# Optimization experiments

Measured on AMD Instinct MI355X. Metric: run time of the kernel, lower is better.

## Reference

```python
import jax, jax.numpy as jnp
import numpy as np

NEG = 0.2  # LeakyReLU slope

def lrelu(x):
    return jnp.where(x >= 0, x, NEG * x)

def conv2d(x, w, pad):
    return jax.lax.conv_general_dilated(x, w, (1, 1), [(pad, pad), (pad, pad)],
                                        dimension_numbers=('NCHW', 'OIHW', 'NCHW'))

def maxpool2(x):
    return jax.lax.reduce_window(x, -jnp.inf, jax.lax.max, (1, 1, 2, 2), (1, 1, 2, 2), 'VALID')

def batchnorm(x, g, b, eps=1e-5):
    m = jnp.mean(x, axis=(0, 2, 3), keepdims=True)
    v = jnp.var(x, axis=(0, 2, 3), keepdims=True)
    return (x - m) / jnp.sqrt(v + eps) * g[None, :, None, None] + b[None, :, None, None]

def features(x, cw1, bg1, bb1, cw2, bg2, bb2, cw3, bg3, bb3, cw4, bg4, bb4):
    x = maxpool2(lrelu(batchnorm(conv2d(x, cw1, 1), bg1, bb1)))
    x = maxpool2(lrelu(batchnorm(conv2d(x, cw2, 1), bg2, bb2)))
    x = lrelu(batchnorm(conv2d(x, cw3, 1), bg3, bb3))
    x = lrelu(batchnorm(conv2d(x, cw4, 1), bg4, bb4))
    return x  # [B,64,16,16]

def mhsa(x, wq, bq, wk, bk, wv, bv, rel_h, rel_w, ln_g, ln_b, heads=4):
    B, C, W, H = x.shape
    d, hw = C // heads, W * H
    def proj(w, b):
        return (jnp.einsum('oc,bchw->bohw', w, x) + b[None, :, None, None]).reshape(B, heads, d, hw)
    q, k, v = proj(wq, bq), proj(wk, bk), proj(wv, bv)
    cc = jnp.einsum('bhdi,bhdj->bhij', q, k)                 # content-content
    pos = (rel_h + rel_w).reshape(heads, d, hw)              # relative position bias
    cp = jnp.einsum('hdi,bhdj->bhij', pos, q)                # content-position
    attn = jax.nn.softmax(cc + cp, axis=-1)
    out = jnp.einsum('bhdj,bhij->bhdi', v, attn).reshape(B, C, W, H)
    m = jnp.mean(out, axis=(1, 2, 3), keepdims=True)
    va = jnp.var(out, axis=(1, 2, 3), keepdims=True)
    out = (out - m) / jnp.sqrt(va + 1e-5) * ln_g[None] + ln_b[None]
    return out + x

def cbam(x, cw1, cb1, cw2, cb2, sw, sb):
    avg, mx = jnp.mean(x, axis=(2, 3)), jnp.max(x, axis=(2, 3))
    def exc(f):
        return jnp.einsum('oc,bc->bo', cw2, jax.nn.relu(jnp.einsum('oc,bc->bo', cw1, f) + cb1)) + cb2
    x = jax.nn.sigmoid(exc(avg) + exc(mx))[:, :, None, None] * x
    sf = jnp.stack([jnp.mean(x, axis=1), jnp.max(x, axis=1)], axis=1)  # [B,2,H,W]
    sa = jax.nn.sigmoid(conv2d(sf, sw, 3) + sb[None, :, None, None])
    return sa * x

def sa_module(x, mh, cb):
    return mhsa(x, *mh) + cbam(x, *cb) + x

def setup_inputs() -> dict:
    key = jax.random.key(0)
    ks = jax.random.split(key, 24)
    rn = lambda k, s, sc=1.0: jax.random.normal(k, s, dtype=jnp.float32) * sc
    inp = {
        'input1': rn(ks[0], (64, 1, 64, 64)),
        'input2': rn(ks[1], (5, 5, 1, 64, 64)),
        'conv1_w': rn(ks[2], (64, 1, 3, 3), 0.3),
        'bn1_g': jnp.ones(64), 'bn1_b': jnp.zeros(64),
        'conv2_w': rn(ks[3], (64, 64, 3, 3), 0.05),
        'bn2_g': jnp.ones(64), 'bn2_b': jnp.zeros(64),
        'conv3_w': rn(ks[4], (64, 64, 3, 3), 0.05),
        'bn3_g': jnp.ones(64), 'bn3_b': jnp.zeros(64),
        'conv4_w': rn(ks[5], (64, 64, 3, 3), 0.05),
        'bn4_g': jnp.ones(64), 'bn4_b': jnp.zeros(64),
        'wq': rn(ks[6], (64, 64), 0.12), 'bq': rn(ks[7], (64,), 0.01),
        'wk': rn(ks[8], (64, 64), 0.12), 'bk': rn(ks[9], (64,), 0.01),
        'wv': rn(ks[10], (64, 64), 0.12), 'bv': rn(ks[11], (64,), 0.01),
        'rel_h': rn(ks[12], (1, 4, 16, 1, 16)),
        'rel_w': rn(ks[13], (1, 4, 16, 16, 1)),
        'ln_g': jnp.ones((64, 16, 16)), 'ln_b': jnp.zeros((64, 16, 16)),
        'ca_w1': rn(ks[14], (4, 64), 0.15), 'ca_b1': jnp.zeros(4),
        'ca_w2': rn(ks[15], (64, 4), 0.15), 'ca_b2': jnp.zeros(64),
        'sa_w': rn(ks[16], (1, 2, 7, 7), 0.1), 'sa_b': jnp.zeros(1),
        'cls_w': rn(ks[17], (256,), 0.05),
    }
    return inp

def reference(input1, input2, conv1_w, bn1_g, bn1_b, conv2_w, bn2_g, bn2_b,
              conv3_w, bn3_g, bn3_b, conv4_w, bn4_g, bn4_b,
              wq, bq, wk, bk, wv, bv, rel_h, rel_w, ln_g, ln_b,
              ca_w1, ca_b1, ca_w2, ca_b2, sa_w, sa_b, cls_w):
    fa = (conv1_w, bn1_g, bn1_b, conv2_w, bn2_g, bn2_b, conv3_w, bn3_g, bn3_b, conv4_w, bn4_g, bn4_b)
    mh = (wq, bq, wk, bk, wv, bv, rel_h, rel_w, ln_g, ln_b)
    cb = (ca_w1, ca_b1, ca_w2, ca_b2, sa_w, sa_b)
    q = sa_module(features(input1, *fa), mh, cb)                      # [B,64,16,16]
    S = jax.vmap(lambda imgs: sa_module(features(imgs, *fa), mh, cb))(input2)  # [ncls,shot,64,16,16]
    ncls, shot = input2.shape[0], input2.shape[1]
    B, C, Hh, Ww = q.shape
    hw = Hh * Ww
    # per-class covariance over channels (CovaBlock.cal_covariance)
    X = S.transpose(0, 2, 1, 3, 4).reshape(ncls, C, shot * hw)
    Xc = X - jnp.mean(X, axis=2, keepdims=True)
    cov = jnp.einsum('ncm,ndm->ncd', Xc, Xc) / (hw * shot - 1)        # [ncls,C,C]
    # query similarity: diag(q^T Cov q) done as fused quadratic form
    Q = q.reshape(B, C, hw)
    Qn = Q / jnp.linalg.norm(Q, axis=2, keepdims=True)
    sim = jnp.einsum('bci,jcd,bdi->bji', Qn, cov, Qn)                 # [B,ncls,hw]
    # classifier: LeakyReLU -> Dropout(eval=identity) -> Conv1d(k=hw, stride=hw, no bias)
    out = jnp.einsum('bjk,k->bj', lrelu(sim), cls_w)
    return out
```

## Files before the change

kernel.cpp:

```cpp
#include <hip/hip_runtime.h>
#include <hip/hip_bf16.h>

__device__ __forceinline__ float lrelu(float x){ return x >= 0.f ? x : 0.2f*x; }
__device__ __forceinline__ float sigm(float x){ return 1.f/(1.f+__expf(-x)); }

typedef short short8 __attribute__((ext_vector_type(8)));
typedef float f32x16 __attribute__((ext_vector_type(16)));

static constexpr size_t OFF_X0    = 0;
static constexpr size_t OFF_POS   = 475712;
static constexpr size_t OFF_WQT   = 492096;
static constexpr size_t OFF_STATS = 504384;
static constexpr size_t OFF_P1    = 507456;
static constexpr size_t OFF_P2    = 7092224;
static constexpr size_t OFF_RES   = 10714688;
static constexpr size_t OFF_MU    = 12172864;
static constexpr size_t OFF_COV   = 12173184;
static constexpr size_t OFF_SIM   = 12193664;
static constexpr size_t OFF_R1    = 12275584;
static constexpr size_t OFF_C2    = OFF_R1;
static constexpr size_t OFF_ATP   = OFF_R1;
static constexpr size_t OFF_C3    = OFF_R1 + 5832704;
static constexpr size_t OFF_C4    = OFF_R1 + 8749056;
static constexpr size_t OFF_CKV   = OFF_R1 + 10207232;
static constexpr size_t OFF_MHRAW = OFF_R1 + 14581760;
static constexpr size_t OFF_QN    = OFF_R1 + 17543680;
static constexpr size_t OFF_WH    = OFF_R1 + 21737984;
static constexpr size_t OFF_WL    = OFF_WH + 18432;

__device__ __forceinline__ int bn_group(int img){ return (img < 64) ? 0 : (1 + (img-64)/5); }

__device__ __forceinline__ void bn_ab(const float* __restrict__ sums, int g, int c, float n,
                                      float gw, float bw, float& a, float& b)
{
    const float sum = sums[(g*64+c)*2], ss = sums[(g*64+c)*2+1];
    const float m = sum/n;
    const float var = fmaxf(ss/n - m*m, 0.f);
    const float istd = 1.f/sqrtf(var + 1e-5f);
    a = gw*istd;
    b = bw - m*a;
}

__global__ __launch_bounds__(256) void prep_k(const float* __restrict__ in1, const float* __restrict__ in2,
        const float* __restrict__ relh, const float* __restrict__ relw,
        const float* __restrict__ wq, const float* __restrict__ wk, const float* __restrict__ wv,
        const float* __restrict__ cw2,
        float* __restrict__ ws)
{
    int idx = blockIdx.x*256 + threadIdx.x;
    if (idx < 364544) { ws[OFF_X0+idx] = (idx < 262144 ? in1[idx] : in2[idx-262144]); return; }
    idx -= 364544;
    if (idx < 16384) {
        const int h = idx>>12, r = idx&4095, i = r>>4, d = r&15;
        ws[OFF_POS+idx] = relh[h*256 + d*16 + (i&15)] + relw[h*256 + d*16 + (i>>4)];
        return;
    }
    idx -= 16384;
    if (idx < 12288) {
        const int s = idx/4096, r = idx%4096, c = r>>6, o = r&63;
        const float* wp = (s==0)?wq:((s==1)?wk:wv);
        ws[OFF_WQT+idx] = wp[o*64 + c];
        return;
    }
    idx -= 12288;
    if (idx < 3072) { ws[OFF_STATS+idx] = 0.f; return; }
    idx -= 3072;
    if (idx < 20480) { ws[OFF_COV+idx] = 0.f; return; }
    idx -= 20480;
    if (idx < 36864) {
        const int och = idx/576, r = idx%576, cin = r/9, k9 = r%9;
        const float v = cw2[idx];
        __hip_bfloat16 hb = __float2bfloat16(v);
        const float hv = __bfloat162float(hb);
        __hip_bfloat16 lb = __float2bfloat16(v - hv);
        unsigned short* WH = (unsigned short*)(ws + OFF_WH);
        unsigned short* WL = (unsigned short*)(ws + OFF_WL);
        const int d = k9*4096 + och*64 + cin;
        WH[d] = *(unsigned short*)&hb;
        WL[d] = *(unsigned short*)&lb;
        return;
    }
    idx -= 36864;
    if (idx < 751872) {
        const int img = idx/8448, r = idx%8448;
        const int pos = r>>6, d = r&63;
        int ypad, xpad;
        if (pos < 68){ ypad = (pos<34)?0:33; xpad = (pos<34)?pos:(pos-34); }
        else { const int q = pos-68; ypad = 1 + (q>>1); xpad = (q&1)*33; }
        ws[OFF_P1 + (((size_t)img*34 + ypad)*34 + xpad)*64 + d] = 0.f;
    }
}

template<int H, int W, int CIN, int CH, int OCB, int PT, bool STORE, bool INBN>
__global__ __launch_bounds__(256) void conv3x3_k(const float* __restrict__ in,
                                                 const float* __restrict__ wt,
                                                 float* __restrict__ out,
                                                 float* __restrict__ bnsum,
                                                 const float* __restrict__ isums,
                                                 const float* __restrict__ igw,
                                                 const float* __restrict__ ibw,
                                                 int ihw)
{
    constexpr int P = W + 1;
    constexpr int PLANE = H * P;
    constexpr int HW = H * W;
    constexpr int PASSES = HW / (256 * PT);
    constexpr int NLD = CH * HW / 256;
    __shared__ float lds[CH * PLANE];
    __shared__ float redS[OCB*4], redQ[OCB*4];
    __shared__ float abA[64], abB[64];
    const int img = blockIdx.x;
    const int och0 = blockIdx.y * OCB;
    const int t = threadIdx.x;

    if constexpr (INBN) {
        if (t < CIN) {
            const int gi = bn_group(img);
            const float nin = (float)(((gi==0)?64:5) * ihw);
            float a, b;
            bn_ab(isums, gi, t, nin, igw[t], ibw[t], a, b);
            abA[t]=a; abB[t]=b;
        }
        __syncthreads();
    }

    float acc[PASSES][OCB][PT];
#pragma unroll
    for (int a=0;a<PASSES;a++)
#pragma unroll
      for (int o=0;o<OCB;o++)
#pragma unroll
        for (int p=0;p<PT;p++) acc[a][o][p]=0.f;

    for (int idx = t; idx < CH*HW; idx += 256) {
        const int c = idx / HW, p = idx % HW;
        float v = in[((size_t)img*CIN + c)*HW + p];
        if constexpr (INBN) v = lrelu(abA[c]*v + abB[c]);
        lds[c*PLANE + (p/W)*P + (p%W)] = v;
    }
    __syncthreads();

    for (int cc0 = 0; cc0 < CIN; cc0 += CH) {
        float pre[(CIN > CH) ? NLD : 1];
        if constexpr (CIN > CH) {
            if (cc0 + CH < CIN) {
#pragma unroll
                for (int j=0;j<NLD;j++){
                    const int idx = j*256 + t;
                    const int c = idx / HW, p = idx % HW;
                    pre[j] = in[((size_t)img*CIN + cc0 + CH + c)*HW + p];
                }
            }
        }
        for (int c = 0; c < CH; ++c) {
            float wr[OCB][9];
#pragma unroll
            for (int o=0;o<OCB;o++)
#pragma unroll
              for (int k=0;k<9;k++)
                wr[o][k] = wt[((size_t)(och0+o)*CIN + (cc0+c))*9 + k];
            const float* Lc = lds + c*PLANE;
#pragma unroll
            for (int ps=0; ps<PASSES; ++ps) {
                const int px0 = (ps*256 + t)*PT;
                const int y = px0 / W, x0 = px0 % W;
#pragma unroll
                for (int ky=0; ky<3; ++ky) {
                    const int yy = y + ky - 1;
                    if (yy >= 0 && yy < H) {
                        const float* Lr = Lc + yy*P;
                        float r[PT+2];
                        r[0] = (x0 > 0) ? Lr[x0-1] : 0.f;
#pragma unroll
                        for (int k2=0;k2<PT;k2++) r[k2+1] = Lr[x0+k2];
                        r[PT+1] = (x0+PT < W) ? Lr[x0+PT] : 0.f;
#pragma unroll
                        for (int p=0;p<PT;p++)
#pragma unroll
                          for (int kx=0;kx<3;kx++) {
                              const float v = r[p+kx];
#pragma unroll
                              for (int o=0;o<OCB;o++)
                                  acc[ps][o][p] += v * wr[o][ky*3+kx];
                          }
                    }
                }
            }
        }
        if constexpr (CIN > CH) {
            if (cc0 + CH < CIN) {
                __syncthreads();
#pragma unroll
                for (int j=0;j<NLD;j++){
                    const int idx = j*256 + t;
                    const int c = idx / HW, p = idx % HW;
                    float v = pre[j];
                    if constexpr (INBN) v = lrelu(abA[cc0+CH+c]*v + abB[cc0+CH+c]);
                    lds[c*PLANE + (p/W)*P + (p%W)] = v;
                }
                __syncthreads();
            }
        }
    }
    if constexpr (STORE) {
#pragma unroll
        for (int ps=0; ps<PASSES; ++ps) {
            const int px0 = (ps*256 + t)*PT;
#pragma unroll
            for (int o=0;o<OCB;o++)
#pragma unroll
              for (int p=0;p<PT;p++)
                out[((size_t)img*64 + och0+o)*HW + px0 + p] = acc[ps][o][p];
        }
    }
    const int g = bn_group(img);
    const int wv = t >> 6;
#pragma unroll
    for (int o=0;o<OCB;o++){
        float s=0.f, ss=0.f;
#pragma unroll
        for (int ps=0;ps<PASSES;ps++)
#pragma unroll
          for (int p=0;p<PT;p++){ const float v=acc[ps][o][p]; s+=v; ss+=v*v; }
#pragma unroll
        for (int off=32; off>0; off>>=1){ s += __shfl_xor(s, off); ss += __shfl_xor(ss, off); }
        if ((t&63)==0){ redS[o*4+wv]=s; redQ[o*4+wv]=ss; }
    }
    __syncthreads();
    if (t < OCB*2){
        const int o = t>>1, metric = t&1;
        const float v = metric ? (redQ[o*4]+redQ[o*4+1]+redQ[o*4+2]+redQ[o*4+3])
                               : (redS[o*4]+redS[o*4+1]+redS[o*4+2]+redS[o*4+3]);
        atomicAdd(&bnsum[(g*64 + och0+o)*2 + metric], v);
    }
}

__global__ __launch_bounds__(256) void bnpoolconv1_k(const float* __restrict__ x0,
        const float* __restrict__ cw, const float* __restrict__ sums,
        const float* __restrict__ gw, const float* __restrict__ bw,
        unsigned short* __restrict__ p1p)
{
    __shared__ float xl[10*64];
    const int img = blockIdx.x, band = blockIdx.y, t = threadIdx.x;
    const int oy0 = band*4;
    const float* xp = x0 + (size_t)img*4096;
    for (int idx=t; idx<640; idx+=256){
        const int iy = idx>>6, ix = idx&63;
        const int gy = 2*oy0 - 1 + iy;
        xl[idx] = (gy>=0 && gy<64) ? xp[gy*64+ix] : 0.f;
    }
    const int g = bn_group(img);
    const float n = (float)(((g==0)?64:5) * 4096);
    __syncthreads();
    const int p = t>>1, half = t&1;
    const int ly = p>>5, ox = p&31;
    float r[4][4];
#pragma unroll
    for (int dy=0;dy<4;dy++){
        const float* Lr = xl + (2*ly+dy)*64;
#pragma unroll
        for (int dx=0;dx<4;dx++){
            const int xx = 2*ox-1+dx;
            r[dy][dx] = (xx>=0 && xx<64) ? Lr[xx] : 0.f;
        }
    }
    short8 hv[4], lv[4];
#pragma unroll
    for (int o=0;o<32;o++){
        const int och = half*32 + o;
        float w[9];
#pragma unroll
        for (int k=0;k<9;k++) w[k] = cw[och*9+k];
        float a, b;
        bn_ab(sums, g, och, n, gw[och], bw[och], a, b);
        float best = -1e30f;
#pragma unroll
        for (int sy=0;sy<2;sy++)
#pragma unroll
          for (int sx=0;sx<2;sx++){
            float s=0.f;
#pragma unroll
            for (int ky=0;ky<3;ky++)
#pragma unroll
              for (int kx=0;kx<3;kx++) s += r[sy+ky][sx+kx]*w[ky*3+kx];
            best = fmaxf(best, lrelu(a*s+b));
          }
        __hip_bfloat16 hb = __float2bfloat16(best);
        const float hf = __bfloat162float(hb);
        __hip_bfloat16 lb = __float2bfloat16(best - hf);
        hv[o>>3][o&7] = (short)*(unsigned short*)&hb;
        lv[o>>3][o&7] = (short)*(unsigned short*)&lb;
    }
    const size_t base = ((((size_t)img*34 + (oy0+ly) + 1)*34) + ox + 1)*128 + half*32;
#pragma unroll
    for (int j=0;j<4;j++){
        *(short8*)(p1p + base + j*8)      = hv[j];
        *(short8*)(p1p + base + 64 + j*8) = lv[j];
    }
}

__global__ __launch_bounds__(256) void conv2mfma_k(const unsigned short* __restrict__ p1p,
        const unsigned short* __restrict__ whi, const unsigned short* __restrict__ wlo,
        float* __restrict__ c2)
{
    __shared__ __align__(16) unsigned short Bx[136*128];
    const int img = blockIdx.x, rowblk = blockIdx.y;
    const int t = threadIdx.x;
    {
        const unsigned short* src = p1p + (((size_t)img*34 + rowblk*2)*34)*128;
        for (int idx=t; idx<2176; idx+=256){
            const int pos = idx>>4, sub = idx&15;
            const short8 v = *(const short8*)(src + pos*128 + sub*8);
            *(short8*)(Bx + pos*128 + ((sub ^ (pos&7))<<3)) = v;
        }
    }
    __syncthreads();
    const int lane = t & 63, wv = t >> 6;
    const int mt = wv & 1, ntp = wv >> 1;
    const int m = lane & 31, kg = lane >> 5;
    f32x16 acc;
#pragma unroll
    for (int r=0;r<16;r++) acc[r]=0.f;

#pragma unroll
    for (int ky=0; ky<3; ky++){
#pragma unroll
      for (int kx=0; kx<3; kx++){
        const int s = ky*3 + kx;
        const unsigned short* wh = whi + ((s*64 + mt*32 + m)<<6) + kg*8;
        const unsigned short* wl = wlo + ((s*64 + mt*32 + m)<<6) + kg*8;
        const int pos = (ntp+ky)*34 + m + kx;
        const int pb  = pos << 7;
        const int sw  = (pos & 7) << 3;
#pragma unroll
        for (int ch=0; ch<4; ch++){
            const short8 ah = *(const short8*)(wh + ch*16);
            const short8 al = *(const short8*)(wl + ch*16);
            const short8 bh = *(const short8*)(Bx + pb + ((ch*16 + (kg<<3)) ^ sw));
            const short8 bl = *(const short8*)(Bx + pb + (64 + ((ch*16 + (kg<<3)) ^ sw)));
            acc = __builtin_amdgcn_mfma_f32_32x32x16_bf16(ah, bh, acc, 0,0,0);
            acc = __builtin_amdgcn_mfma_f32_32x32x16_bf16(al, bh, acc, 0,0,0);
            acc = __builtin_amdgcn_mfma_f32_32x32x16_bf16(ah, bl, acc, 0,0,0);
        }
      }
    }
    const int py = rowblk*2 + ntp;
    float* co = c2 + ((size_t)img*64)*1024 + py*32 + m;
#pragma unroll
    for (int r=0; r<16; r++){
        const int och = mt*32 + (r&3) + 8*(r>>2) + 4*kg;
        co[(size_t)och*1024] = acc[r];
    }
}

__global__ __launch_bounds__(256) void bnstats2_k(const float* __restrict__ in, float* __restrict__ sums)
{
    __shared__ float rs[4], rq[4];
    const int img = blockIdx.x, c = blockIdx.y, t = threadIdx.x;
    const float4 v = ((const float4*)(in + ((size_t)img*64 + c)*1024))[t];
    float s = v.x+v.y+v.z+v.w;
    float q = v.x*v.x+v.y*v.y+v.z*v.z+v.w*v.w;
#pragma unroll
    for (int off=32; off>0; off>>=1){ s += __shfl_xor(s, off); q += __shfl_xor(q, off); }
    if ((t&63)==0){ rs[t>>6]=s; rq[t>>6]=q; }
    __syncthreads();
    if (t==0){
        const int g = bn_group(img);
        atomicAdd(&sums[(g*64+c)*2],   rs[0]+rs[1]+rs[2]+rs[3]);
        atomicAdd(&sums[(g*64+c)*2+1], rq[0]+rq[1]+rq[2]+rq[3]);
    }
}

template<int H, int W>
__global__ __launch_bounds__(256) void bnpool_k(const float* __restrict__ in, const float* __restrict__ sums,
                                 const float* __restrict__ gw, const float* __restrict__ bw,
                                 float* __restrict__ out)
{
    const int img = blockIdx.x, c = blockIdx.y, t = threadIdx.x;
    const int g = bn_group(img);
    const float n = (float)(((g==0)?64:5) * H * W);
    float a, b;
    bn_ab(sums, g, c, n, gw[c], bw[c], a, b);
    constexpr int W2=W/2, HW=H*W, N2=(H/2)*W2;
    const float* pl = in + ((size_t)img*64 + c)*HW;
    float* po = out + ((size_t)img*64 + c)*N2;
    for (int opx=t; opx<N2; opx+=256) {
        const int oy=opx/W2, ox=opx%W2;
        const float* q = pl + (2*oy)*W + 2*ox;
        const float v0=lrelu(a*q[0]+b), v1=lrelu(a*q[1]+b), v2=lrelu(a*q[W]+b), v3=lrelu(a*q[W+1]+b);
        po[opx] = fmaxf(fmaxf(v0,v1),fmaxf(v2,v3));
    }
}

__global__ __launch_bounds__(256) void proj_k(const float* __restrict__ c4, const float* __restrict__ wT,
               const float* __restrict__ bq, const float* __restrict__ bk, const float* __restrict__ bv,
               const float* __restrict__ sums4, const float* __restrict__ gw4, const float* __restrict__ bw4,
               float* __restrict__ ckv)
{
    __shared__ float xl[64*256];
    const int img = blockIdx.x, s = blockIdx.y, t = threadIdx.x;
    const int gi = bn_group(img);
    const float nin = (float)(((gi==0)?64:5) * 256);
    {
        const float4* in4 = (const float4*)(c4 + (size_t)img*16384);
        float4* xl4 = (float4*)xl;
        for (int i=t; i<4096; i+=256){
            float4 v = in4[i];
            const int c = i>>6;
            float a, b;
            bn_ab(sums4, gi, c, nin, gw4[c], bw4[c], a, b);
            v.x=lrelu(a*v.x+b); v.y=lrelu(a*v.y+b); v.z=lrelu(a*v.z+b); v.w=lrelu(a*v.w+b);
            xl4[i] = v;
        }
    }
    const float* bias = (s==0)?bq:((s==1)?bk:bv);
    const int sofs = (s==0)?16:((s==1)?0:32);
    const float* wp = wT + s*4096;
    const int o0 = (t>>4)*4, i0 = (t&15)*16;
    const int h = o0>>4, d0 = o0&15;
    __syncthreads();
    float acc[4][16];
    float b0[4];
#pragma unroll
    for (int o=0;o<4;o++) b0[o]=bias[o0+o];
#pragma unroll
    for (int o=0;o<4;o++)
#pragma unroll
      for (int i=0;i<16;i++) acc[o][i]=b0[o];
    for (int c=0;c<64;c++){
        const float4 w4 = *(const float4*)(wp + c*64 + o0);
        const float* xr = xl + c*256 + i0;
#pragma unroll
        for (int k=0;k<4;k++){
            const float4 x4 = *(const float4*)(xr + 4*k);
            acc[0][4*k+0]+=w4.x*x4.x; acc[0][4*k+1]+=w4.x*x4.y; acc[0][4*k+2]+=w4.x*x4.z; acc[0][4*k+3]+=w4.x*x4.w;
            acc[1][4*k+0]+=w4.y*x4.x; acc[1][4*k+1]+=w4.y*x4.y; acc[1][4*k+2]+=w4.y*x4.z; acc[1][4*k+3]+=w4.y*x4.w;
            acc[2][4*k+0]+=w4.z*x4.x; acc[2][4*k+1]+=w4.z*x4.y; acc[2][4*k+2]+=w4.z*x4.z; acc[2][4*k+3]+=w4.z*x4.w;
            acc[3][4*k+0]+=w4.w*x4.x; acc[3][4*k+1]+=w4.w*x4.y; acc[3][4*k+2]+=w4.w*x4.z; acc[3][4*k+3]+=w4.w*x4.w;
        }
    }
#pragma unroll
    for (int ii=0;ii<16;ii++){
        const float4 v = make_float4(acc[0][ii],acc[1][ii],acc[2][ii],acc[3][ii]);
        *(float4*)(ckv + (((size_t)img*4 + h)*256 + i0+ii)*48 + sofs + d0) = v;
    }
}

__global__ __launch_bounds__(256) void attnp_k(const float* __restrict__ ckv, const float* __restrict__ pos,
                               float* __restrict__ part)
{
    const int img = blockIdx.x, h = blockIdx.y, jc = blockIdx.z, i = threadIdx.x;
    const size_t jb = (((size_t)img*4 + h)*256)*48;
    float areg[32];
    {
        const float* myrow = ckv + jb + (size_t)i*48;
#pragma unroll
        for (int k=0;k<4;k++) *(float4*)&areg[4*k]    = *(const float4*)(myrow + 16 + 4*k);
#pragma unroll
        for (int k=0;k<4;k++) *(float4*)&areg[16+4*k] = *(const float4*)(pos + h*4096 + i*16 + 4*k);
    }
    float mrun = -1e30f, l = 0.f;
    float accv[16];
#pragma unroll
    for (int d=0;d<16;d++) accv[d]=0.f;

    const int jend = jc*64 + 64;
    for (int j0=jc*64; j0<jend; j0+=2){
        const float* r0 = ckv + jb + (size_t)j0*48;
        const float* r1 = r0 + 48;
        float s0a=0.f, s0b=0.f, s1a=0.f, s1b=0.f;
#pragma unroll
        for (int dd=0; dd<16; ++dd){
            s0a += areg[2*dd]  *r0[2*dd];
            s0b += areg[2*dd+1]*r0[2*dd+1];
            s1a += areg[2*dd]  *r1[2*dd];
            s1b += areg[2*dd+1]*r1[2*dd+1];
        }
        const float s0 = s0a+s0b, s1 = s1a+s1b;
        const float mnew = fmaxf(mrun, fmaxf(s0,s1));
        const float al = __expf(mrun - mnew);
        const float e0 = __expf(s0 - mnew), e1 = __expf(s1 - mnew);
        mrun = mnew;
        l = l*al + e0 + e1;
        const float* v0 = r0 + 32;
        const float* v1 = r1 + 32;
#pragma unroll
        for (int d=0;d<16;d++) accv[d] = accv[d]*al + e0*v0[d] + e1*v1[d];
    }
    float* pp = part + ((((size_t)img*4 + h)*4 + jc)*18)*256;
    pp[i]       = mrun;
    pp[256 + i] = l;
#pragma unroll
    for (int d=0;d<16;d++) pp[(2+d)*256 + i] = accv[d];
}

__global__ __launch_bounds__(256) void attnm_k(const float* __restrict__ part, float* __restrict__ mhraw)
{
    const int img = blockIdx.x, h = blockIdx.y, i = threadIdx.x;
    const float* pb = part + (((size_t)img*4 + h)*4*18)*256;
    float mc[4], lc[4];
#pragma unroll
    for (int c=0;c<4;c++){ mc[c] = pb[c*4608 + i]; lc[c] = pb[c*4608 + 256 + i]; }
    const float ms = fmaxf(fmaxf(mc[0],mc[1]), fmaxf(mc[2],mc[3]));
    float wgt[4]; float ls = 0.f;
#pragma unroll
    for (int c=0;c<4;c++){ wgt[c] = __expf(mc[c]-ms); ls += wgt[c]*lc[c]; }
    const float rl = 1.f/ls;
#pragma unroll
    for (int d=0;d<16;d++){
        float v = 0.f;
#pragma unroll
        for (int c=0;c<4;c++) v += wgt[c]*pb[c*4608 + (2+d)*256 + i];
        mhraw[((size_t)img*64 + h*16 + d)*256 + i] = v*rl;
    }
}

__global__ __launch_bounds__(256) void post_k(const float* __restrict__ mhraw,
        const float* __restrict__ lng, const float* __restrict__ lnb,
        const float* __restrict__ c4,
        const float* __restrict__ sums4, const float* __restrict__ gw4, const float* __restrict__ bw4,
        const float* __restrict__ w1, const float* __restrict__ b1,
        const float* __restrict__ w2, const float* __restrict__ b2,
        const float* __restrict__ sw, const float* __restrict__ sb,
        float* __restrict__ res)
{
    __shared__ float r1[256], r2[256];
    __shared__ float favg[64], fmx[64], z1s[8], ca[64];
    __shared__ float sf[512];
    __shared__ float wl[98];
    __shared__ float mh_s[2];
    __shared__ float aA[64], aB[64];
    __shared__ float sa_l[256];
    const int img = blockIdx.x, t = threadIdx.x;
    const float* mb  = mhraw + (size_t)img*16384;
    const float* fbr = c4    + (size_t)img*16384;

    if (t<64){
        const int gi = bn_group(img);
        const float nin = (float)(((gi==0)?64:5) * 256);
        float a, b;
        bn_ab(sums4, gi, t, nin, gw4[t], bw4[t], a, b);
        aA[t]=a; aB[t]=b;
    }
    if (t<98) wl[t] = sw[t];

    {
        const float4* mb4 = (const float4*)mb;
        float s=0.f, ss=0.f;
        for (int i=t; i<4096; i+=256){
            const float4 v = mb4[i];
            s  += v.x+v.y+v.z+v.w;
            ss += v.x*v.x+v.y*v.y+v.z*v.z+v.w*v.w;
        }
        r1[t]=s; r2[t]=ss; __syncthreads();
        for (int st=128;st>0;st>>=1){ if(t<st){r1[t]+=r1[t+st]; r2[t]+=r2[t+st];} __syncthreads(); }
        if (t==0){
            const float m = r1[0]/16384.f;
            const float var = fmaxf(r2[0]/16384.f - m*m, 0.f);
            mh_s[0]=m; mh_s[1]=1.f/sqrtf(var+1e-5f);
        }
    }
    {
        const int c = t>>2, part = t&3;
        const float a = aA[c], b = aB[c];
        const float4* p4 = (const float4*)(fbr + c*256 + part*64);
        float s=0.f, mx=-1e30f;
        for (int k=0;k<16;k++){
            const float4 v = p4[k];
            const float f0=lrelu(a*v.x+b), f1=lrelu(a*v.y+b), f2=lrelu(a*v.z+b), f3=lrelu(a*v.w+b);
            s += f0+f1+f2+f3;
            mx = fmaxf(mx, fmaxf(fmaxf(f0,f1),fmaxf(f2,f3)));
        }
        __syncthreads();
        r1[t]=s; r2[t]=mx;
        __syncthreads();
        if (t<64){
            favg[t] = (r1[t*4]+r1[t*4+1]+r1[t*4+2]+r1[t*4+3])/256.f;
            fmx[t]  = fmaxf(fmaxf(r2[t*4],r2[t*4+1]),fmaxf(r2[t*4+2],r2[t*4+3]));
        }
    }
    __syncthreads();
    if (t<8){
        const int which = t>>2, o = t&3;
        const float* f = which? fmx : favg;
        float z = b1[o];
        for (int c=0;c<64;c++) z += w1[o*64+c]*f[c];
        z1s[t] = fmaxf(z, 0.f);
    }
    __syncthreads();
    if (t<64){
        float z = 2.f*b2[t];
#pragma unroll
        for (int k=0;k<4;k++) z += w2[t*4+k]*(z1s[k]+z1s[4+k]);
        ca[t] = sigm(z);
    }
    __syncthreads();
    {
        float s=0.f, mx=-1e30f;
        for (int c=0;c<64;c++){
            const float fv = lrelu(aA[c]*fbr[c*256+t] + aB[c]);
            const float v = ca[c]*fv;
            s += v; mx = fmaxf(mx, v);
        }
        sf[t]     = s/64.f;
        sf[256+t] = mx;
    }
    __syncthreads();
    {
        float sacc = sb[0];
        const int y = t>>4, x = t&15;
        for (int ch=0; ch<2; ++ch)
          for (int ky=0; ky<7; ++ky){
            const int yy = y+ky-3;
            if (yy<0||yy>=16) continue;
            for (int kx=0; kx<7; ++kx){
                const int xx = x+kx-3;
                if (xx<0||xx>=16) continue;
                sacc += sf[ch*256 + yy*16 + xx]*wl[ch*49 + ky*7 + kx];
            }
          }
        sa_l[t] = sigm(sacc);
    }
    __syncthreads();
    {
        const int q = t & 63;
        const int cb = t >> 6;
        const float m = mh_s[0], istd = mh_s[1];
        const float4* mb4 = (const float4*)mb;
        const float4* fb4 = (const float4*)fbr;
        const float4* lg4 = (const float4*)lng;
        const float4* lb4 = (const float4*)lnb;
        float4* res4 = (float4*)(res + (size_t)img*16384);
        const float sa0=sa_l[4*q], sa1=sa_l[4*q+1], sa2=sa_l[4*q+2], sa3=sa_l[4*q+3];
#pragma unroll 4
        for (int cc=0; cc<16; ++cc){
            const int c = cb*16 + cc;
            const int i4 = c*64 + q;
            const float4 mv = mb4[i4], fv = fb4[i4], gv = lg4[i4], bv = lb4[i4];
            const float a = aA[c], b = aB[c], cf = ca[c];
            float4 r;
            r.x = (mv.x-m)*istd*gv.x + bv.x + lrelu(a*fv.x+b)*(2.f + sa0*cf);
            r.y = (mv.y-m)*istd*gv.y + bv.y + lrelu(a*fv.y+b)*(2.f + sa1*cf);
            r.z = (mv.z-m)*istd*gv.z + bv.z + lrelu(a*fv.z+b)*(2.f + sa2*cf);
            r.w = (mv.w-m)*istd*gv.w + bv.w + lrelu(a*fv.w+b)*(2.f + sa3*cf);
            res4[i4] = r;
        }
    }
}

__global__ __launch_bounds__(256) void covmu_k(const float* __restrict__ res, float* __restrict__ mu)
{
    __shared__ float r1[256];
    const int n = blockIdx.x, c = blockIdx.y, t = threadIdx.x;
    float s=0.f;
    for (int sh=0; sh<5; ++sh)
        s += res[((size_t)(64 + n*5 + sh)*64 + c)*256 + t];
    r1[t]=s; __syncthreads();
    for (int st=128;st>0;st>>=1){ if(t<st) r1[t]+=r1[t+st]; __syncthreads(); }
    if (t==0) mu[n*64+c] = r1[0]/1280.f;
}

__global__ __launch_bounds__(256) void cov_k(const float* __restrict__ res, const float* __restrict__ mu,
                                             float* __restrict__ cov)
{
    __shared__ float Xl[64*129];
    const int n = blockIdx.x, by = blockIdx.y, sh = blockIdx.z, t = threadIdx.x;
    const int c = by*16 + (t>>4);
    const int d0 = (t&15)*4;
    float acc[4] = {0.f,0.f,0.f,0.f};
    for (int half=0; half<2; ++half){
        __syncthreads();
        for (int idx=t; idx<8192; idx+=256){
            const int ch = idx>>7, p = idx&127;
            Xl[ch*129+p] = res[((size_t)(64+n*5+sh)*64 + ch)*256 + half*128 + p] - mu[n*64+ch];
        }
        __syncthreads();
        for (int p=0;p<128;p++){
            const float xc = Xl[c*129+p];
#pragma unroll
            for (int k=0;k<4;k++) acc[k] += xc*Xl[(d0+k)*129+p];
        }
    }
#pragma unroll
    for (int k=0;k<4;k++) atomicAdd(&cov[((size_t)n*64 + c)*64 + d0+k], acc[k]*(1.f/1279.f));
}

__global__ __launch_bounds__(64) void qn_k(const float* __restrict__ res, float* __restrict__ qn)
{
    const int b = blockIdx.x, c = blockIdx.y, t = threadIdx.x;
    const size_t base = ((size_t)b*64 + c)*256;
    const float4 v = *(const float4*)(res + base + t*4);
    float ss = v.x*v.x + v.y*v.y + v.z*v.z + v.w*v.w;
#pragma unroll
    for (int off=32; off>0; off>>=1) ss += __shfl_xor(ss, off);
    const float inv = 1.f/sqrtf(ss);
    float4 o; o.x=v.x*inv; o.y=v.y*inv; o.z=v.z*inv; o.w=v.w*inv;
    *(float4*)(qn + base + t*4) = o;
}

__global__ __launch_bounds__(256) void sim_k(const float* __restrict__ qn, const float* __restrict__ cov,
                                             float* __restrict__ sim)
{
    __shared__ float covj[64*65];
    __shared__ float Vl[64*68];
    __shared__ float simred[320];
    const int b = blockIdx.x, iq = blockIdx.y, t = threadIdx.x;
    const int i0g = iq*64;
    for (int idx=t; idx<4096; idx+=256){
        const int c = idx>>6, il = idx&63;
        Vl[c*68+il] = qn[((size_t)b*64+c)*256 + i0g + il];
    }
    for (int idx=t; idx<320; idx+=256) simred[idx]=0.f;
    const int c0 = (t>>4)*4, i0 = (t&15)*4;
    for (int j=0;j<5;j++){
        __syncthreads();
        for (int idx=t; idx<4096; idx+=256)
            covj[(idx>>6)*65 + (idx&63)] = cov[(size_t)j*4096 + idx];
        __syncthreads();
        float pt[4][4];
#pragma unroll
        for (int a=0;a<4;a++)
#pragma unroll
          for (int bb=0;bb<4;bb++) pt[a][bb]=0.f;
        for (int d=0; d<64; ++d){
            const float4 vv = *(const float4*)&Vl[d*68 + i0];
            float cw[4];
#pragma unroll
            for (int cc=0;cc<4;cc++) cw[cc] = covj[(c0+cc)*65 + d];
#pragma unroll
            for (int cc=0;cc<4;cc++){
                pt[cc][0] += cw[cc]*vv.x;
                pt[cc][1] += cw[cc]*vv.y;
                pt[cc][2] += cw[cc]*vv.z;
                pt[cc][3] += cw[cc]*vv.w;
            }
        }
#pragma unroll
        for (int ii=0;ii<4;ii++){
            float s = 0.f;
#pragma unroll
            for (int cc=0;cc<4;cc++) s += pt[cc][ii]*Vl[(c0+cc)*68 + i0+ii];
            atomicAdd(&simred[j*64 + i0 + ii], s);
        }
    }
    __syncthreads();
    for (int idx=t; idx<320; idx+=256){
        const int j = idx>>6, il = idx&63;
        sim[((size_t)b*5 + j)*256 + i0g + il] = simred[idx];
    }
}

__global__ __launch_bounds__(256) void cls_k(const float* __restrict__ sim, const float* __restrict__ cw,
                                             float* __restrict__ out)
{
    __shared__ float red[256];
    const int b = blockIdx.x, t = threadIdx.x;
    const float w = cw[t];
    for (int j=0;j<5;j++){
        const float v = sim[((size_t)b*5 + j)*256 + t];
        red[t] = lrelu(v)*w;
        __syncthreads();
        for (int st=128;st>0;st>>=1){ if(t<st) red[t]+=red[t+st]; __syncthreads(); }
        if (t==0) out[b*5+j] = red[0];
        __syncthreads();
    }
}

extern "C" void kernel_launch(void* const* d_in, const int* in_sizes, int n_in,
                              void* d_out, int out_size, void* d_ws, size_t ws_size,
                              hipStream_t stream)
{
    const float* IN[31];
    for (int i=0;i<31;i++) IN[i] = (const float*)d_in[i];
    float* W = (float*)d_ws;
    float* OUT = (float*)d_out;
    const unsigned short* WHp = (const unsigned short*)(W + OFF_WH);
    const unsigned short* WLp = (const unsigned short*)(W + OFF_WL);
    unsigned short* P1P = (unsigned short*)(W + OFF_P1);

    prep_k<<<4709,256,0,stream>>>(IN[0],IN[1],IN[20],IN[21],IN[14],IN[16],IN[18],IN[5],W);

    conv3x3_k<64,64,1,1,4,4,false,false><<<dim3(89,16),256,0,stream>>>(W+OFF_X0, IN[2], nullptr, W+OFF_STATS, nullptr,nullptr,nullptr,0);
    bnpoolconv1_k<<<dim3(89,8),256,0,stream>>>(W+OFF_X0, IN[2], W+OFF_STATS, IN[3], IN[4], P1P);

    conv2mfma_k<<<dim3(89,16),256,0,stream>>>(P1P, WHp, WLp, W+OFF_C2);
    bnstats2_k<<<dim3(89,64),256,0,stream>>>(W+OFF_C2, W+OFF_STATS+768);
    bnpool_k<32,32><<<dim3(89,64),256,0,stream>>>(W+OFF_C2, W+OFF_STATS+768, IN[6], IN[7], W+OFF_P2);

    conv3x3_k<16,16,64,16,8,1,true,false><<<dim3(89,8),256,0,stream>>>(W+OFF_P2, IN[8], W+OFF_C3, W+OFF_STATS+1536, nullptr,nullptr,nullptr,0);

    conv3x3_k<16,16,64,16,8,1,true,true><<<dim3(89,8),256,0,stream>>>(W+OFF_C3, IN[11], W+OFF_C4, W+OFF_STATS+2304,
                                                                      W+OFF_STATS+1536, IN[9], IN[10], 256);

    proj_k<<<dim3(89,3),256,0,stream>>>(W+OFF_C4, W+OFF_WQT, IN[15], IN[17], IN[19],
                                        W+OFF_STATS+2304, IN[12], IN[13], W+OFF_CKV);
    attnp_k<<<dim3(89,4,4),256,0,stream>>>(W+OFF_CKV, W+OFF_POS, W+OFF_ATP);
    attnm_k<<<dim3(89,4),256,0,stream>>>(W+OFF_ATP, W+OFF_MHRAW);

    post_k<<<89,256,0,stream>>>(W+OFF_MHRAW, IN[22], IN[23], W+OFF_C4,
                                W+OFF_STATS+2304, IN[12], IN[13],
                                IN[24], IN[25], IN[26], IN[27], IN[28], IN[29], W+OFF_RES);

    covmu_k<<<dim3(5,64),256,0,stream>>>(W+OFF_RES, W+OFF_MU);
    cov_k<<<dim3(5,4,5),256,0,stream>>>(W+OFF_RES, W+OFF_MU, W+OFF_COV);
    qn_k<<<dim3(64,64),64,0,stream>>>(W+OFF_RES, W+OFF_QN);
    sim_k<<<dim3(64,4),256,0,stream>>>(W+OFF_QN, W+OFF_COV, W+OFF_SIM);
    cls_k<<<64,256,0,stream>>>(W+OFF_SIM, IN[30], OUT);
}
```

Before: 545.5 us.

## Run conv3 and conv4 on bf16 MFMA with split-precision packed inputs

Replaces the scalar FP32 direct 3x3 convolutions for layers 3 and 4 with an MFMA kernel. It uses hi/lo bf16 splitting of weights and activations (three MFMAs per step) to keep close to FP32 accuracy. The BN+pool stage after conv2 and a new BN+LReLU stage after conv3 now write padded NHWC bf16 hi/lo packs. BN statistics are spread over 8 partial slots to reduce atomic contention. Prep work grows to convert the extra weights and zero the padding borders, and the split-bf16 scheme may lose slight accuracy compared with FP32.

```diff
diff --git a/kernel.cpp b/kernel.cpp
--- a/kernel.cpp
+++ b/kernel.cpp
@@ -13,6 +13,12 @@
 static constexpr size_t OFF_STATS = 504384;
 static constexpr size_t OFF_P1    = 507456;
 static constexpr size_t OFF_P2    = 7092224;
+static constexpr size_t OFF_S3    = 8937728;
+static constexpr size_t OFF_S4    = 8943872;
+static constexpr size_t OFF_WH3   = 8950016;
+static constexpr size_t OFF_WL3   = 8968448;
+static constexpr size_t OFF_WH4   = 8986880;
+static constexpr size_t OFF_WL4   = 9005312;
 static constexpr size_t OFF_RES   = 10714688;
 static constexpr size_t OFF_MU    = 12172864;
 static constexpr size_t OFF_COV   = 12173184;
@@ -23,6 +29,7 @@
 static constexpr size_t OFF_C3    = OFF_R1 + 5832704;
 static constexpr size_t OFF_C4    = OFF_R1 + 8749056;
 static constexpr size_t OFF_CKV   = OFF_R1 + 10207232;
+static constexpr size_t OFF_C3P   = OFF_R1 + 10207232;
 static constexpr size_t OFF_MHRAW = OFF_R1 + 14581760;
 static constexpr size_t OFF_QN    = OFF_R1 + 17543680;
 static constexpr size_t OFF_WH    = OFF_R1 + 21737984;
@@ -41,10 +48,26 @@
     b = bw - m*a;
 }
 
+__device__ __forceinline__ void bn_ab_s8(const float* __restrict__ sums, int g, int c, float n,
+                                         float gw, float bw, float& a, float& b)
+{
+    float sum = 0.f, ss = 0.f;
+#pragma unroll
+    for (int s=0;s<8;s++){
+        sum += sums[s*768 + (g*64+c)*2];
+        ss  += sums[s*768 + (g*64+c)*2 + 1];
+    }
+    const float m = sum/n;
+    const float var = fmaxf(ss/n - m*m, 0.f);
+    const float istd = 1.f/sqrtf(var + 1e-5f);
+    a = gw*istd;
+    b = bw - m*a;
+}
+
 __global__ __launch_bounds__(256) void prep_k(const float* __restrict__ in1, const float* __restrict__ in2,
         const float* __restrict__ relh, const float* __restrict__ relw,
         const float* __restrict__ wq, const float* __restrict__ wk, const float* __restrict__ wv,
-        const float* __restrict__ cw2,
+        const float* __restrict__ cw2, const float* __restrict__ cw3, const float* __restrict__ cw4,
         float* __restrict__ ws)
 {
     int idx = blockIdx.x*256 + threadIdx.x;
@@ -67,20 +90,26 @@
     idx -= 3072;
     if (idx < 20480) { ws[OFF_COV+idx] = 0.f; return; }
     idx -= 20480;
-    if (idx < 36864) {
-        const int och = idx/576, r = idx%576, cin = r/9, k9 = r%9;
-        const float v = cw2[idx];
+    if (idx < 12288) { ws[OFF_S3+idx] = 0.f; return; }
+    idx -= 12288;
+    if (idx < 110592) {
+        const int which = idx / 36864, r0 = idx - which*36864;
+        const int och = r0/576, rr = r0%576, cin = rr/9, k9 = rr%9;
+        const float* cwp = (which==0)?cw2:((which==1)?cw3:cw4);
+        const float v = cwp[r0];
         __hip_bfloat16 hb = __float2bfloat16(v);
         const float hv = __bfloat162float(hb);
         __hip_bfloat16 lb = __float2bfloat16(v - hv);
-        unsigned short* WH = (unsigned short*)(ws + OFF_WH);
-        unsigned short* WL = (unsigned short*)(ws + OFF_WL);
+        const size_t oh = (which==0)?OFF_WH:((which==1)?OFF_WH3:OFF_WH4);
+        const size_t ol = (which==0)?OFF_WL:((which==1)?OFF_WL3:OFF_WL4);
+        unsigned short* WH = (unsigned short*)(ws + oh);
+        unsigned short* WL = (unsigned short*)(ws + ol);
         const int d = k9*4096 + och*64 + cin;
         WH[d] = *(unsigned short*)&hb;
         WL[d] = *(unsigned short*)&lb;
         return;
     }
-    idx -= 36864;
+    idx -= 110592;
     if (idx < 751872) {
         const int img = idx/8448, r = idx%8448;
         const int pos = r>>6, d = r&63;
@@ -88,6 +117,26 @@
         if (pos < 68){ ypad = (pos<34)?0:33; xpad = (pos<34)?pos:(pos-34); }
         else { const int q = pos-68; ypad = 1 + (q>>1); xpad = (q&1)*33; }
         ws[OFF_P1 + (((size_t)img*34 + ypad)*34 + xpad)*64 + d] = 0.f;
+        return;
+    }
+    idx -= 751872;
+    if (idx < 387328) {
+        const int img = idx/4352, r = idx%4352;
+        const int pos = r>>6, d = r&63;
+        int ypad, xpad;
+        if (pos < 36){ ypad = (pos<18)?0:17; xpad = (pos<18)?pos:(pos-18); }
+        else { const int q = pos-36; ypad = 1 + (q>>1); xpad = (q&1)*17; }
+        ws[OFF_P2 + (((size_t)img*18 + ypad)*18 + xpad)*64 + d] = 0.f;
+        return;
+    }
+    idx -= 387328;
+    if (idx < 387328) {
+        const int img = idx/4352, r = idx%4352;
+        const int pos = r>>6, d = r&63;
+        int ypad, xpad;
+        if (pos < 36){ ypad = (pos<18)?0:17; xpad = (pos<18)?pos:(pos-18); }
+        else { const int q = pos-36; ypad = 1 + (q>>1); xpad = (q&1)*17; }
+        ws[OFF_C3P + (((size_t)img*18 + ypad)*18 + xpad)*64 + d] = 0.f;
     }
 }
 
@@ -371,24 +420,152 @@
     }
 }
 
-template<int H, int W>
-__global__ __launch_bounds__(256) void bnpool_k(const float* __restrict__ in, const float* __restrict__ sums,
-                                 const float* __restrict__ gw, const float* __restrict__ bw,
-                                 float* __restrict__ out)
-{
-    const int img = blockIdx.x, c = blockIdx.y, t = threadIdx.x;
+__global__ __launch_bounds__(256) void bnpool_pack_k(const float* __restrict__ c2,
+        const float* __restrict__ sums, const float* __restrict__ gw, const float* __restrict__ bw,
+        unsigned short* __restrict__ p2p)
+{
+    __shared__ float aA[64], aB[64];
+    const int img = blockIdx.x, cb = blockIdx.y, t = threadIdx.x;
     const int g = bn_group(img);
-    const float n = (float)(((g==0)?64:5) * H * W);
-    float a, b;
-    bn_ab(sums, g, c, n, gw[c], bw[c], a, b);
-    constexpr int W2=W/2, HW=H*W, N2=(H/2)*W2;
-    const float* pl = in + ((size_t)img*64 + c)*HW;
-    float* po = out + ((size_t)img*64 + c)*N2;
-    for (int opx=t; opx<N2; opx+=256) {
-        const int oy=opx/W2, ox=opx%W2;
-        const float* q = pl + (2*oy)*W + 2*ox;
-        const float v0=lrelu(a*q[0]+b), v1=lrelu(a*q[1]+b), v2=lrelu(a*q[W]+b), v3=lrelu(a*q[W+1]+b);
-        po[opx] = fmaxf(fmaxf(v0,v1),fmaxf(v2,v3));
+    if (t < 64){
+        const float n = (float)(((g==0)?64:5) * 1024);
+        float a, b;
+        bn_ab(sums, g, t, n, gw[t], bw[t], a, b);
+        aA[t]=a; aB[t]=b;
+    }
+    __syncthreads();
+    const int oy = t>>4, ox = t&15;
+    const float* pim = c2 + (size_t)img*65536 + (size_t)cb*32768 + oy*64 + ox*2;
+    short8 hv[4], lv[4];
+#pragma unroll
+    for (int j8=0;j8<4;j8++){
+#pragma unroll
+      for (int e=0;e<8;e++){
+        const int j = j8*8 + e;
+        const int c = cb*32 + j;
+        const float* pl = pim + (size_t)j*1024;
+        const float2 u = *(const float2*)pl;
+        const float2 v = *(const float2*)(pl + 32);
+        const float a = aA[c], b = aB[c];
+        const float best = fmaxf(fmaxf(lrelu(a*u.x+b), lrelu(a*u.y+b)),
+                                 fmaxf(lrelu(a*v.x+b), lrelu(a*v.y+b)));
+        __hip_bfloat16 hb = __float2bfloat16(best);
+        const float hf = __bfloat162float(hb);
+        __hip_bfloat16 lb = __float2bfloat16(best - hf);
+        hv[j8][e] = (short)*(unsigned short*)&hb;
+        lv[j8][e] = (short)*(unsigned short*)&lb;
+      }
+    }
+    unsigned short* dst = p2p + (((size_t)img*18 + oy+1)*18 + ox+1)*128 + cb*32;
+#pragma unroll
+    for (int j=0;j<4;j++){
+        *(short8*)(dst + j*8)      = hv[j];
+        *(short8*)(dst + 64 + j*8) = lv[j];
+    }
+}
+
+__global__ __launch_bounds__(256) void conv16mfma_k(const unsigned short* __restrict__ pack,
+        const unsigned short* __restrict__ whi, const unsigned short* __restrict__ wlo,
+        float* __restrict__ out, float* __restrict__ bnsum)
+{
+    __shared__ __align__(16) unsigned short Bx[108*128];
+    const int img = blockIdx.x, rowblk = blockIdx.y;
+    const int t = threadIdx.x;
+    {
+        const unsigned short* src = pack + (((size_t)img*18 + rowblk*4)*18)*128;
+        for (int idx=t; idx<1728; idx+=256){
+            const int pos = idx>>4, sub = idx&15;
+            const short8 v = *(const short8*)(src + pos*128 + sub*8);
+            *(short8*)(Bx + pos*128 + ((sub ^ (pos&7))<<3)) = v;
+        }
+    }
+    __syncthreads();
+    const int lane = t & 63, wv = t >> 6;
+    const int mt = wv & 1, np = wv >> 1;
+    const int m = lane & 31, kg = lane >> 5;
+    f32x16 acc;
+#pragma unroll
+    for (int r=0;r<16;r++) acc[r]=0.f;
+
+#pragma unroll
+    for (int ky=0; ky<3; ky++){
+#pragma unroll
+      for (int kx=0; kx<3; kx++){
+        const int s = ky*3 + kx;
+        const unsigned short* wh = whi + ((s*64 + mt*32 + m)<<6) + kg*8;
+        const unsigned short* wl = wlo + ((s*64 + mt*32 + m)<<6) + kg*8;
+        const int pos = (np*2 + (m>>4) + ky)*18 + (m&15) + kx;
+        const int pb  = pos << 7;
+        const int sw  = (pos & 7) << 3;
+#pragma unroll
+        for (int ch=0; ch<4; ch++){
+            const short8 ah = *(const short8*)(wh + ch*16);
+            const short8 al = *(const short8*)(wl + ch*16);
+            const short8 bh = *(const short8*)(Bx + pb + ((ch*16 + (kg<<3)) ^ sw));
+            const short8 bl = *(const short8*)(Bx + pb + (64 + ((ch*16 + (kg<<3)) ^ sw)));
+            acc = __builtin_amdgcn_mfma_f32_32x32x16_bf16(ah, bh, acc, 0,0,0);
+            acc = __builtin_amdgcn_mfma_f32_32x32x16_bf16(al, bh, acc, 0,0,0);
+            acc = __builtin_amdgcn_mfma_f32_32x32x16_bf16(ah, bl, acc, 0,0,0);
+        }
+      }
+    }
+    float* co = out + (size_t)img*16384 + rowblk*64 + np*32 + m;
+#pragma unroll
+    for (int r=0; r<16; r++){
+        const int och = mt*32 + (r&3) + 8*(r>>2) + 4*kg;
+        co[(size_t)och*256] = acc[r];
+    }
+    const int g = bn_group(img);
+    float* bs = bnsum + (rowblk*2 + np)*768;
+#pragma unroll
+    for (int r=0; r<16; r++){
+        float sv = acc[r], qv = acc[r]*acc[r];
+#pragma unroll
+        for (int off=16; off>0; off>>=1){ sv += __shfl_xor(sv, off); qv += __shfl_xor(qv, off); }
+        if (m == r){
+            const int och = mt*32 + (r&3) + 8*(r>>2) + 4*kg;
+            atomicAdd(&bs[(g*64+och)*2],   sv);
+            atomicAdd(&bs[(g*64+och)*2+1], qv);
+        }
+    }
+}
+
+__global__ __launch_bounds__(256) void c3pack_k(const float* __restrict__ c3,
+        const float* __restrict__ s3, const float* __restrict__ gw, const float* __restrict__ bw,
+        unsigned short* __restrict__ c3p)
+{
+    __shared__ float aA[64], aB[64];
+    const int img = blockIdx.x, cb = blockIdx.y, t = threadIdx.x;
+    const int g = bn_group(img);
+    if (t < 64){
+        const float n = (float)(((g==0)?64:5) * 256);
+        float a, b;
+        bn_ab_s8(s3, g, t, n, gw[t], bw[t], a, b);
+        aA[t]=a; aB[t]=b;
+    }
+    __syncthreads();
+    const float* pim = c3 + (size_t)img*16384 + (size_t)cb*8192 + t;
+    short8 hv[4], lv[4];
+#pragma unroll
+    for (int j8=0;j8<4;j8++){
+#pragma unroll
+      for (int e=0;e<8;e++){
+        const int j = j8*8 + e;
+        const int c = cb*32 + j;
+        const float v = lrelu(aA[c]*pim[(size_t)j*256] + aB[c]);
+        __hip_bfloat16 hb = __float2bfloat16(v);
+        const float hf = __bfloat162float(hb);
+        __hip_bfloat16 lb = __float2bfloat16(v - hf);
+        hv[j8][e] = (short)*(unsigned short*)&hb;
+        lv[j8][e] = (short)*(unsigned short*)&lb;
+      }
+    }
+    const int oy = t>>4, ox = t&15;
+    unsigned short* dst = c3p + (((size_t)img*18 + oy+1)*18 + ox+1)*128 + cb*32;
+#pragma unroll
+    for (int j=0;j<4;j++){
+        *(short8*)(dst + j*8)      = hv[j];
+        *(short8*)(dst + 64 + j*8) = lv[j];
     }
 }
 
@@ -408,7 +585,7 @@
             float4 v = in4[i];
             const int c = i>>6;
             float a, b;
-            bn_ab(sums4, gi, c, nin, gw4[c], bw4[c], a, b);
+            bn_ab_s8(sums4, gi, c, nin, gw4[c], bw4[c], a, b);
             v.x=lrelu(a*v.x+b); v.y=lrelu(a*v.y+b); v.z=lrelu(a*v.z+b); v.w=lrelu(a*v.w+b);
             xl4[i] = v;
         }
@@ -539,7 +716,7 @@
         const int gi = bn_group(img);
         const float nin = (float)(((gi==0)?64:5) * 256);
         float a, b;
-        bn_ab(sums4, gi, t, nin, gw4[t], bw4[t], a, b);
+        bn_ab_s8(sums4, gi, t, nin, gw4[t], bw4[t], a, b);
         aA[t]=a; aB[t]=b;
     }
     if (t<98) wl[t] = sw[t];
@@ -774,31 +951,38 @@
     for (int i=0;i<31;i++) IN[i] = (const float*)d_in[i];
     float* W = (float*)d_ws;
     float* OUT = (float*)d_out;
-    const unsigned short* WHp = (const unsigned short*)(W + OFF_WH);
-    const unsigned short* WLp = (const unsigned short*)(W + OFF_WL);
+    const unsigned short* WHp  = (const unsigned short*)(W + OFF_WH);
+    const unsigned short* WLp  = (const unsigned short*)(W + OFF_WL);
+    const unsigned short* WH3p = (const unsigned short*)(W + OFF_WH3);
+    const unsigned short* WL3p = (const unsigned short*)(W + OFF_WL3);
+    const unsigned short* WH4p = (const unsigned short*)(W + OFF_WH4);
+    const unsigned short* WL4p = (const unsigned short*)(W + OFF_WL4);
     unsigned short* P1P = (unsigned short*)(W + OFF_P1);
-
-    prep_k<<<4709,256,0,stream>>>(IN[0],IN[1],IN[20],IN[21],IN[14],IN[16],IN[18],IN[5],W);
+    unsigned short* P2P = (unsigned short*)(W + OFF_P2);
+    unsigned short* C3P = (unsigned short*)(W + OFF_C3P);
+
+    prep_k<<<8072,256,0,stream>>>(IN[0],IN[1],IN[20],IN[21],IN[14],IN[16],IN[18],
+                                  IN[5],IN[8],IN[11],W);
 
     conv3x3_k<64,64,1,1,4,4,false,false><<<dim3(89,16),256,0,stream>>>(W+OFF_X0, IN[2], nullptr, W+OFF_STATS, nullptr,nullptr,nullptr,0);
     bnpoolconv1_k<<<dim3(89,8),256,0,stream>>>(W+OFF_X0, IN[2], W+OFF_STATS, IN[3], IN[4], P1P);
 
     conv2mfma_k<<<dim3(89,16),256,0,stream>>>(P1P, WHp, WLp, W+OFF_C2);
     bnstats2_k<<<dim3(89,64),256,0,stream>>>(W+OFF_C2, W+OFF_STATS+768);
-    bnpool_k<32,32><<<dim3(89,64),256,0,stream>>>(W+OFF_C2, W+OFF_STATS+768, IN[6], IN[7], W+OFF_P2);
-
-    conv3x3_k<16,16,64,16,8,1,true,false><<<dim3(89,8),256,0,stream>>>(W+OFF_P2, IN[8], W+OFF_C3, W+OFF_STATS+1536, nullptr,nullptr,nullptr,0);
-
-    conv3x3_k<16,16,64,16,8,1,true,true><<<dim3(89,8),256,0,stream>>>(W+OFF_C3, IN[11], W+OFF_C4, W+OFF_STATS+2304,
-                                                                      W+OFF_STATS+1536, IN[9], IN[10], 256);
+    bnpool_pack_k<<<dim3(89,2),256,0,stream>>>(W+OFF_C2, W+OFF_STATS+768, IN[6], IN[7], P2P);
+
+    conv16mfma_k<<<dim3(89,4),256,0,stream>>>(P2P, WH3p, WL3p, W+OFF_C3, W+OFF_S3);
+    c3pack_k<<<dim3(89,2),256,0,stream>>>(W+OFF_C3, W+OFF_S3, IN[9], IN[10], C3P);
+
+    conv16mfma_k<<<dim3(89,4),256,0,stream>>>(C3P, WH4p, WL4p, W+OFF_C4, W+OFF_S4);
 
     proj_k<<<dim3(89,3),256,0,stream>>>(W+OFF_C4, W+OFF_WQT, IN[15], IN[17], IN[19],
-                                        W+OFF_STATS+2304, IN[12], IN[13], W+OFF_CKV);
+                                        W+OFF_S4, IN[12], IN[13], W+OFF_CKV);
     attnp_k<<<dim3(89,4,4),256,0,stream>>>(W+OFF_CKV, W+OFF_POS, W+OFF_ATP);
     attnm_k<<<dim3(89,4),256,0,stream>>>(W+OFF_ATP, W+OFF_MHRAW);
 
     post_k<<<89,256,0,stream>>>(W+OFF_MHRAW, IN[22], IN[23], W+OFF_C4,
-                                W+OFF_STATS+2304, IN[12], IN[13],
+                                W+OFF_S4, IN[12], IN[13],
                                 IN[24], IN[25], IN[26], IN[27], IN[28], IN[29], W+OFF_RES);
 
     covmu_k<<<dim3(5,64),256,0,stream>>>(W+OFF_RES, W+OFF_MU);
```

Measured after the change: 527.6 us. 1.03x faster.
